# Kernel tuning notes

Hardware: AMD Instinct MI355X
Metric: run time of the kernel (lower is better)

Reference implementation:

```python
import jax, jax.numpy as jnp
import numpy as np

EPS = 1e-12

def setup_inputs() -> dict:
    key = jax.random.key(0)
    k1, k2, k3, k4, k5 = jax.random.split(key, 5)
    n, C, B = 8, 1024, 2048
    X = jax.random.normal(k1, (n, C, B), dtype=jnp.float32)
    # xavier_uniform bound for square [C, C] weight
    bound = float(np.sqrt(6.0 / (C + C)))
    Wk_w = jax.random.uniform(k2, (C, C), dtype=jnp.float32, minval=-bound, maxval=bound)
    Wq_w = jax.random.uniform(k3, (C, C), dtype=jnp.float32, minval=-bound, maxval=bound)
    # nn.Linear default bias init: U(-1/sqrt(C), 1/sqrt(C))
    bb = 1.0 / float(np.sqrt(C))
    Wk_b = jax.random.uniform(k4, (C,), dtype=jnp.float32, minval=-bb, maxval=bb)
    Wq_b = jax.random.uniform(k5, (C,), dtype=jnp.float32, minval=-bb, maxval=bb)
    return {"X": X, "Wk_w": Wk_w, "Wk_b": Wk_b, "Wq_w": Wq_w, "Wq_b": Wq_b}

def reference(X, Wk_w, Wk_b, Wq_w, Wq_b):
    # X: [n, C, B]; weights: [C, C]; biases: [C]
    K = jnp.einsum('oc,ncb->nob', Wk_w, X) + Wk_b[:, None]   # [n, C, B]
    Q = jnp.einsum('oc,ncb->nob', Wq_w, X) + Wq_b[:, None]   # [n, C, B]
    DK2 = jnp.sum(K * K, axis=1)                              # [n, B]
    DQ2 = jnp.sum(Q * Q, axis=1)                              # [n, B]
    DQK = jnp.sqrt(jnp.maximum(DQ2[:, :, None] * DK2[:, None, :], EPS))  # [n, B, B]
    Y = jnp.einsum('ncb,nck->nbk', Q, K) / DQK                # [n, B, B] cosine-like scores
    SM = jax.nn.softmax(Y, axis=1)                            # softmax over query axis (dim=1)
    Z = jnp.einsum('ncb,nbk->nck', X, SM)                     # [n, C, B]
    return Z
```

## Files before the change

kernel.cpp:

```cpp
#include <hip/hip_runtime.h>
#include <hip/hip_bf16.h>

typedef __bf16 v8bf __attribute__((ext_vector_type(8)));
typedef __bf16 v4bf __attribute__((ext_vector_type(4)));
typedef float  v4f  __attribute__((ext_vector_type(4)));

#define AS1 __attribute__((address_space(1)))
#define AS3 __attribute__((address_space(3)))

static __device__ __forceinline__ void gload_lds16(const void* g, void* l) {
  __builtin_amdgcn_global_load_lds((const AS1 void*)g, (AS3 void*)l, 16, 0, 0);
}

__global__ __launch_bounds__(256)
void cvt_bf16(const float* __restrict__ in, __bf16* __restrict__ out, long n) {
  const long i = ((long)blockIdx.x * 256 + threadIdx.x) * 4;
  if (i >= n) return;
  v4f v = *(const v4f*)&in[i];
  v4bf o;
#pragma unroll
  for (int u = 0; u < 4; ++u) o[u] = (__bf16)v[u];
  *(v4bf*)&out[i] = o;
}

__global__ __launch_bounds__(256)
void cvt_transpose(const float* __restrict__ X, __bf16* __restrict__ XT) {
  __shared__ float t[64][65];
  const int b0 = blockIdx.x * 64, c0 = blockIdx.y * 64;
  const long n = blockIdx.z;
  const float* Xp = X + n * (1024L * 2048);
  __bf16* Tp = XT + n * (2048L * 1024);
  const int tid = threadIdx.x;
  const int r16 = tid >> 4, c4 = (tid & 15) * 4;
#pragma unroll
  for (int it = 0; it < 4; ++it) {
    const int r = r16 + it * 16;
    *(v4f*)&t[r][c4] = *(const v4f*)&Xp[(long)(c0 + r) * 2048 + b0 + c4];
  }
  __syncthreads();
  const int rb8 = tid >> 3, c8 = (tid & 7) * 8;
#pragma unroll
  for (int it = 0; it < 2; ++it) {
    const int rb = rb8 + it * 32;
    v8bf o;
#pragma unroll
    for (int u = 0; u < 8; ++u) o[u] = (__bf16)t[c8 + u][rb];
    *(v8bf*)&Tp[(long)(b0 + rb) * 1024 + c0 + c8] = o;
  }
}

#define BAR __builtin_amdgcn_s_barrier()
#define LGKM0 do { asm volatile("s_waitcnt lgkmcnt(0)" ::: "memory"); \
                   __builtin_amdgcn_sched_barrier(0); } while (0)
#define VMW6 do { asm volatile("s_waitcnt vmcnt(6)" ::: "memory"); \
                  __builtin_amdgcn_sched_barrier(0); } while (0)
#define VMW0 do { asm volatile("s_waitcnt vmcnt(0)" ::: "memory"); \
                  __builtin_amdgcn_sched_barrier(0); } while (0)
#define MM(HM, HN) do { \
  __builtin_amdgcn_s_setprio(1); \
  _Pragma("unroll") for (int ks = 0; ks < 2; ++ks) \
  _Pragma("unroll") for (int u = 0; u < 2; ++u) \
  _Pragma("unroll") for (int j = 0; j < 4; ++j) \
    acc[2 * (HM) + u][4 * (HN) + j] = __builtin_amdgcn_mfma_f32_16x16x32_bf16( \
        af[u][ks], bfr[j][ks], acc[2 * (HM) + u][4 * (HN) + j], 0, 0, 0); \
  __builtin_amdgcn_s_setprio(0); } while (0)

template<int KD, int EPI, typename OT>
__global__ __launch_bounds__(512, 2)
void gemm256(const __bf16* __restrict__ Abase, const __bf16* __restrict__ Bbase,
             OT* __restrict__ Obase, const __bf16* __restrict__ bias,
             const float* __restrict__ dk2, const float* __restrict__ dq2,
             long sA, long sB, long sO) {
  __shared__ __align__(128) __bf16 lds[65536];

  const int tid = threadIdx.x;
  const int wave = tid >> 6, lane = tid & 63;
  const int qr = wave >> 1, qc = wave & 1;
  const int fr = lane & 15, q = lane >> 4;
  const int f7 = fr & 7;

  const int n0 = blockIdx.x * 256, m0 = blockIdx.y * 256;
  const long z = blockIdx.z;

  const __bf16* A = Abase + z * sA + (long)m0 * KD;
  const __bf16* B = Bbase + z * sB + (long)n0 * KD;

  const int lrow = wave * 16 + (lane >> 3);
  const int lchunk = ((lane & 7) ^ (lane >> 3)) << 3;
  const __bf16* Alane = A + (long)lrow * KD + lchunk;
  const __bf16* Blane = B + (long)lrow * KD + lchunk;
  const int dbase = wave * 1024;

  auto stage = [&](int kt, int isB, int half) {
    const __bf16* gp = (isB ? Blane : Alane) + (long)(half * 128) * KD + kt * 64;
    __bf16* dp = lds + (kt & 1) * 32768 + isB * 16384 + half * 8192 + dbase;
    gload_lds16(gp, dp);
    gload_lds16(gp + (long)8 * KD, dp + 512);
  };

  v4f acc[4][8];
#pragma unroll
  for (int i = 0; i < 4; ++i)
#pragma unroll
    for (int j = 0; j < 8; ++j) acc[i][j] = {0.f, 0.f, 0.f, 0.f};

  v8bf af[2][2], bfr[4][2];
  auto readA = [&](const __bf16* sa, int hm) {
#pragma unroll
    for (int u = 0; u < 2; ++u) {
      const int rb = (hm * 128 + qr * 32 + u * 16 + fr) * 64;
      af[u][0] = *(const v8bf*)&sa[rb + ((q ^ f7) << 3)];
      af[u][1] = *(const v8bf*)&sa[rb + (((q | 4) ^ f7) << 3)];
    }
  };
  auto readB = [&](const __bf16* sb, int hn) {
#pragma unroll
    for (int j = 0; j < 4; ++j) {
      const int rb = (hn * 128 + qc * 64 + j * 16 + fr) * 64;
      bfr[j][0] = *(const v8bf*)&sb[rb + ((q ^ f7) << 3)];
      bfr[j][1] = *(const v8bf*)&sb[rb + (((q | 4) ^ f7) << 3)];
    }
  };

  constexpr int NT = KD / 64;
  constexpr int NI = NT / 2;
  __bf16* s0 = lds;
  __bf16* s1 = lds + 32768;

  stage(0, 0, 0); stage(0, 1, 0); stage(0, 1, 1); stage(0, 0, 1);
  stage(1, 0, 0); stage(1, 1, 1); stage(1, 0, 1);
  VMW6; BAR;

#pragma unroll 1
  for (int m = 0; m < NI; ++m) {
    const int T1 = 2 * m + 1, T2 = 2 * m + 2, T3 = 2 * m + 3;
    const bool nl = (m != NI - 1);
    readA(s0, 0); readB(s0 + 16384, 0);
    stage(T1, 1, 0);
    BAR; LGKM0; MM(0, 0); BAR;
    readB(s0 + 16384, 1);
    if (nl) stage(T2, 0, 0);
    BAR; LGKM0; MM(0, 1); BAR;
    readA(s0, 1);
    if (nl) stage(T2, 1, 1);
    BAR; LGKM0; MM(1, 1); BAR;
    readB(s0 + 16384, 0);
    if (nl) stage(T2, 0, 1);
    BAR; LGKM0; MM(1, 0);
    if (nl) { VMW6; } else { VMW0; }
    BAR;
    readA(s1, 0); readB(s1 + 16384, 0);
    if (nl) stage(T2, 1, 0);
    BAR; LGKM0; MM(0, 0); BAR;
    readB(s1 + 16384, 1);
    if (nl) stage(T3, 0, 0);
    BAR; LGKM0; MM(0, 1); BAR;
    readA(s1, 1);
    if (nl) stage(T3, 1, 1);
    BAR; LGKM0; MM(1, 1); BAR;
    readB(s1 + 16384, 0);
    if (nl) stage(T3, 0, 1);
    BAR; LGKM0; MM(1, 0);
    if (nl) { VMW6; } else { VMW0; }
    BAR;
  }

  OT* O = Obase + z * sO;
  const int ldo = gridDim.x * 256;
#pragma unroll
  for (int bj = 0; bj < 8; ++bj) {
    const int col = n0 + (bj >> 2) * 128 + qc * 64 + (bj & 3) * 16 + fr;
    float cv = 0.f;
    if (EPI == 0) cv = (float)bias[col];
    if (EPI == 1) cv = dq2[z * 2048 + col];
#pragma unroll
    for (int ai = 0; ai < 4; ++ai) {
      const int row0 = m0 + (ai >> 1) * 128 + qr * 32 + (ai & 1) * 16 + q * 4;
#pragma unroll
      for (int r = 0; r < 4; ++r) {
        float v = acc[ai][bj][r];
        const int row = row0 + r;
        if (EPI == 0) v = fminf(fmaxf(v + cv, -32.f), 32.f);
        if (EPI == 1) {
          v *= rsqrtf(fmaxf(dk2[z * 2048 + row] * cv, 1e-12f));
          v = fminf(fmaxf(v, -4.f), 4.f);
        }
        if (EPI == 2) v = fminf(fmaxf(v, -1.f), 1.f);
        O[(long)row * ldo + col] = (OT)v;
      }
    }
  }
}

__global__ __launch_bounds__(256)
void rownorm2(const __bf16* __restrict__ T, float* __restrict__ out) {
  const int tid = threadIdx.x;
  const long row = (long)blockIdx.y * gridDim.x + blockIdx.x;
  const __bf16* p = T + row * 1024;
  v4bf v = *(const v4bf*)&p[tid * 4];
  float s = 0.f;
#pragma unroll
  for (int u = 0; u < 4; ++u) { float f = (float)v[u]; s += f * f; }
#pragma unroll
  for (int off = 32; off > 0; off >>= 1) s += __shfl_down(s, off);
  __shared__ float red[4];
  if ((tid & 63) == 0) red[tid >> 6] = s;
  __syncthreads();
  if (tid == 0) out[row] = red[0] + red[1] + red[2] + red[3];
}

__global__ __launch_bounds__(256)
void softmax_rows(__bf16* __restrict__ Y) {
  const int tid = threadIdx.x;
  const long row = (long)blockIdx.y * gridDim.x + blockIdx.x;
  __bf16* p = Y + row * 2048;
  v8bf v = *(const v8bf*)&p[tid * 8];
  float f[8];
  float s = 0.f;
#pragma unroll
  for (int u = 0; u < 8; ++u) { f[u] = __expf((float)v[u]); s += f[u]; }
#pragma unroll
  for (int off = 32; off > 0; off >>= 1) s += __shfl_down(s, off);
  __shared__ float red[4];
  __shared__ float stot;
  if ((tid & 63) == 0) red[tid >> 6] = s;
  __syncthreads();
  if (tid == 0) stot = 1.f / (red[0] + red[1] + red[2] + red[3]);
  __syncthreads();
  const float inv = stot;
  v8bf o;
#pragma unroll
  for (int u = 0; u < 8; ++u) o[u] = (__bf16)(f[u] * inv);
  *(v8bf*)&p[tid * 8] = o;
}

extern "C" void kernel_launch(void* const* d_in, const int* in_sizes, int n_in,
                              void* d_out, int out_size, void* d_ws, size_t ws_size,
                              hipStream_t stream) {
  const float* X    = (const float*)d_in[0];
  const float* Wk_w = (const float*)d_in[1];
  const float* Wk_b = (const float*)d_in[2];
  const float* Wq_w = (const float*)d_in[3];
  const float* Wq_b = (const float*)d_in[4];
  float* out = (float*)d_out;

  char* ws = (char*)d_ws;
  __bf16* XT  = (__bf16*)(ws);
  __bf16* Xbf = (__bf16*)(ws);
  __bf16* YT  = (__bf16*)(ws + 33554432L);
  char* aux   = ws + 100663296L;
  float*  DK2   = (float*)(aux);
  float*  DQ2   = (float*)(aux + 65536L);
  __bf16* Wk_bf = (__bf16*)(aux + 131072L);
  __bf16* Wq_bf = (__bf16*)(aux + 131072L + 2097152L);
  __bf16* bk_bf = (__bf16*)(aux + 131072L + 4194304L);
  __bf16* bq_bf = (__bf16*)(aux + 131072L + 4196352L);
  __bf16* KT = (__bf16*)d_out;
  __bf16* QT = (__bf16*)((char*)d_out + 33554432L);

  cvt_bf16<<<1024, 256, 0, stream>>>(Wk_w, Wk_bf, 1048576L);
  cvt_bf16<<<1024, 256, 0, stream>>>(Wq_w, Wq_bf, 1048576L);
  cvt_bf16<<<1, 256, 0, stream>>>(Wk_b, bk_bf, 1024L);
  cvt_bf16<<<1, 256, 0, stream>>>(Wq_b, bq_bf, 1024L);
  cvt_transpose<<<dim3(32, 16, 8), 256, 0, stream>>>(X, XT);
  gemm256<1024, 0, __bf16><<<dim3(4, 8, 8), 512, 0, stream>>>(
      XT, Wk_bf, KT, bk_bf, nullptr, nullptr, 2048L * 1024, 0L, 2048L * 1024);
  gemm256<1024, 0, __bf16><<<dim3(4, 8, 8), 512, 0, stream>>>(
      XT, Wq_bf, QT, bq_bf, nullptr, nullptr, 2048L * 1024, 0L, 2048L * 1024);
  cvt_bf16<<<16384, 256, 0, stream>>>(X, Xbf, 16777216L);
  rownorm2<<<dim3(2048, 8), 256, 0, stream>>>(KT, DK2);
  rownorm2<<<dim3(2048, 8), 256, 0, stream>>>(QT, DQ2);
  gemm256<1024, 1, __bf16><<<dim3(8, 8, 8), 512, 0, stream>>>(
      KT, QT, YT, nullptr, DK2, DQ2, 2048L * 1024, 2048L * 1024, 2048L * 2048);
  softmax_rows<<<dim3(2048, 8), 256, 0, stream>>>(YT);
  gemm256<2048, 2, float><<<dim3(8, 4, 8), 512, 0, stream>>>(
      Xbf, YT, out, nullptr, nullptr, nullptr, 1024L * 2048, 2048L * 2048, 1024L * 2048);
}
```

Measured before the change: 404.7 us.

## Fuse row norms into projection GEMM epilogue with vectorized stores and XCD block remap

Deletes the two rownorm2 kernels. The K and Q projection GEMM epilogues now compute per-row sums of squares and add them into zeroed DK2/DQ2 buffers with shuffle reductions and atomicAdd. MFMA operands are swapped so each lane holds four consecutive columns, which allows 4-wide vector stores and vector loads of bias and dq2. Blocks are also remapped in an XCD-aware interleaved order, and the LDS pipeline is reordered to put the wait ahead of each barrier and drop the trailing barriers. The intent is to remove two full passes over K and Q plus scattered scalar stores, at the cost of atomic contention, norms taken from fp32 values rather than bf16-rounded ones, and a riskier barrier schedule.

```diff
diff --git a/kernel.cpp b/kernel.cpp
--- a/kernel.cpp
+++ b/kernel.cpp
@@ -21,6 +21,13 @@
 #pragma unroll
   for (int u = 0; u < 4; ++u) o[u] = (__bf16)v[u];
   *(v4bf*)&out[i] = o;
+}
+
+__global__ __launch_bounds__(256)
+void zero_f32(float* __restrict__ p, long n) {
+  const long i = ((long)blockIdx.x * 256 + threadIdx.x) * 4;
+  if (i >= n) return;
+  *(v4f*)&p[i] = v4f{0.f, 0.f, 0.f, 0.f};
 }
 
 __global__ __launch_bounds__(256)
@@ -52,24 +59,22 @@
 #define BAR __builtin_amdgcn_s_barrier()
 #define LGKM0 do { asm volatile("s_waitcnt lgkmcnt(0)" ::: "memory"); \
                    __builtin_amdgcn_sched_barrier(0); } while (0)
-#define VMW6 do { asm volatile("s_waitcnt vmcnt(6)" ::: "memory"); \
-                  __builtin_amdgcn_sched_barrier(0); } while (0)
-#define VMW0 do { asm volatile("s_waitcnt vmcnt(0)" ::: "memory"); \
-                  __builtin_amdgcn_sched_barrier(0); } while (0)
+#define VMW(N) do { asm volatile("s_waitcnt vmcnt(" #N ")" ::: "memory"); \
+                    __builtin_amdgcn_sched_barrier(0); } while (0)
 #define MM(HM, HN) do { \
   __builtin_amdgcn_s_setprio(1); \
   _Pragma("unroll") for (int ks = 0; ks < 2; ++ks) \
   _Pragma("unroll") for (int u = 0; u < 2; ++u) \
   _Pragma("unroll") for (int j = 0; j < 4; ++j) \
     acc[2 * (HM) + u][4 * (HN) + j] = __builtin_amdgcn_mfma_f32_16x16x32_bf16( \
-        af[u][ks], bfr[j][ks], acc[2 * (HM) + u][4 * (HN) + j], 0, 0, 0); \
+        bfr[j][ks], af[u][ks], acc[2 * (HM) + u][4 * (HN) + j], 0, 0, 0); \
   __builtin_amdgcn_s_setprio(0); } while (0)
 
 template<int KD, int EPI, typename OT>
 __global__ __launch_bounds__(512, 2)
 void gemm256(const __bf16* __restrict__ Abase, const __bf16* __restrict__ Bbase,
              OT* __restrict__ Obase, const __bf16* __restrict__ bias,
-             const float* __restrict__ dk2, const float* __restrict__ dq2,
+             float* __restrict__ dk2, const float* __restrict__ dq2,
              long sA, long sB, long sO) {
   __shared__ __align__(128) __bf16 lds[65536];
 
@@ -79,9 +84,16 @@
   const int fr = lane & 15, q = lane >> 4;
   const int f7 = fr & 7;
 
-  const int n0 = blockIdx.x * 256, m0 = blockIdx.y * 256;
-  const long z = blockIdx.z;
-
+  const int gx = gridDim.x, gy = gridDim.y;
+  int id = blockIdx.x + gx * (blockIdx.y + gy * blockIdx.z);
+  const int chunk = (gx * gy * gridDim.z) >> 3;
+  id = (id & 7) * chunk + (id >> 3);
+  const int bx = id % gx;
+  const int rem = id / gx;
+  const int by = rem % gy;
+  const long z = rem / gy;
+
+  const int n0 = bx * 256, m0 = by * 256;
   const __bf16* A = Abase + z * sA + (long)m0 * KD;
   const __bf16* B = Bbase + z * sB + (long)n0 * KD;
 
@@ -127,86 +139,99 @@
   __bf16* s0 = lds;
   __bf16* s1 = lds + 32768;
 
-  stage(0, 0, 0); stage(0, 1, 0); stage(0, 1, 1); stage(0, 0, 1);
-  stage(1, 0, 0); stage(1, 1, 1); stage(1, 0, 1);
-  VMW6; BAR;
+  stage(0, 0, 0); stage(0, 1, 0); stage(0, 0, 1); stage(0, 1, 1);
+  stage(1, 1, 0); stage(1, 0, 1); stage(1, 1, 1);
+  VMW(6); BAR;
 
 #pragma unroll 1
   for (int m = 0; m < NI; ++m) {
-    const int T1 = 2 * m + 1, T2 = 2 * m + 2, T3 = 2 * m + 3;
     const bool nl = (m != NI - 1);
+    const int t1 = 2 * m + 1, t2 = 2 * m + 2, t3 = 2 * m + 3;
     readA(s0, 0); readB(s0 + 16384, 0);
-    stage(T1, 1, 0);
-    BAR; LGKM0; MM(0, 0); BAR;
+    stage(t1, 0, 0);
+    LGKM0; BAR; MM(0, 0);
+    readA(s0, 1);
+    if (nl) stage(t2, 1, 0);
+    LGKM0; BAR; MM(1, 0);
     readB(s0 + 16384, 1);
-    if (nl) stage(T2, 0, 0);
-    BAR; LGKM0; MM(0, 1); BAR;
-    readA(s0, 1);
-    if (nl) stage(T2, 1, 1);
-    BAR; LGKM0; MM(1, 1); BAR;
-    readB(s0 + 16384, 0);
-    if (nl) stage(T2, 0, 1);
-    BAR; LGKM0; MM(1, 0);
-    if (nl) { VMW6; } else { VMW0; }
-    BAR;
+    if (nl) stage(t2, 0, 1);
+    LGKM0; BAR; MM(1, 1);
+    readA(s0, 0);
+    if (nl) stage(t2, 1, 1);
+    LGKM0;
+    if (nl) { VMW(6); } else { VMW(0); }
+    BAR; MM(0, 1);
     readA(s1, 0); readB(s1 + 16384, 0);
-    if (nl) stage(T2, 1, 0);
-    BAR; LGKM0; MM(0, 0); BAR;
+    if (nl) stage(t2, 0, 0);
+    LGKM0; BAR; MM(0, 0);
+    readA(s1, 1);
+    if (nl) stage(t3, 1, 0);
+    LGKM0; BAR; MM(1, 0);
     readB(s1 + 16384, 1);
-    if (nl) stage(T3, 0, 0);
-    BAR; LGKM0; MM(0, 1); BAR;
-    readA(s1, 1);
-    if (nl) stage(T3, 1, 1);
-    BAR; LGKM0; MM(1, 1); BAR;
-    readB(s1 + 16384, 0);
-    if (nl) stage(T3, 0, 1);
-    BAR; LGKM0; MM(1, 0);
-    if (nl) { VMW6; } else { VMW0; }
-    BAR;
+    if (nl) stage(t3, 0, 1);
+    LGKM0; BAR; MM(1, 1);
+    readA(s1, 0);
+    if (nl) stage(t3, 1, 1);
+    LGKM0;
+    if (nl) { VMW(6); } else { VMW(0); }
+    BAR; MM(0, 1);
   }
 
   OT* O = Obase + z * sO;
-  const int ldo = gridDim.x * 256;
-#pragma unroll
-  for (int bj = 0; bj < 8; ++bj) {
-    const int col = n0 + (bj >> 2) * 128 + qc * 64 + (bj & 3) * 16 + fr;
-    float cv = 0.f;
-    if (EPI == 0) cv = (float)bias[col];
-    if (EPI == 1) cv = dq2[z * 2048 + col];
-#pragma unroll
-    for (int ai = 0; ai < 4; ++ai) {
-      const int row0 = m0 + (ai >> 1) * 128 + qr * 32 + (ai & 1) * 16 + q * 4;
+  const int ldo = gx * 256;
+#pragma unroll
+  for (int ai = 0; ai < 4; ++ai) {
+    const int row = m0 + (ai >> 1) * 128 + qr * 32 + (ai & 1) * 16 + fr;
+    float rk = 0.f;
+    if (EPI == 1) rk = dk2[z * 2048 + row];
+    float rs = 0.f;
+#pragma unroll
+    for (int bj = 0; bj < 8; ++bj) {
+      const int colb = n0 + (bj >> 2) * 128 + qc * 64 + (bj & 3) * 16 + q * 4;
+      float cv[4];
+      if (EPI == 0) {
+        v4bf bb = *(const v4bf*)&bias[colb];
+#pragma unroll
+        for (int r = 0; r < 4; ++r) cv[r] = (float)bb[r];
+      }
+      if (EPI == 1) {
+        v4f dd = *(const v4f*)&dq2[z * 2048 + colb];
+#pragma unroll
+        for (int r = 0; r < 4; ++r) cv[r] = dd[r];
+      }
+      float vv[4];
 #pragma unroll
       for (int r = 0; r < 4; ++r) {
         float v = acc[ai][bj][r];
-        const int row = row0 + r;
-        if (EPI == 0) v = fminf(fmaxf(v + cv, -32.f), 32.f);
+        if (EPI == 0) {
+          v = fminf(fmaxf(v + cv[r], -32.f), 32.f);
+          rs += v * v;
+        }
         if (EPI == 1) {
-          v *= rsqrtf(fmaxf(dk2[z * 2048 + row] * cv, 1e-12f));
+          v *= rsqrtf(fmaxf(rk * cv[r], 1e-12f));
           v = fminf(fmaxf(v, -4.f), 4.f);
         }
         if (EPI == 2) v = fminf(fmaxf(v, -1.f), 1.f);
-        O[(long)row * ldo + col] = (OT)v;
+        vv[r] = v;
+      }
+      if (sizeof(OT) == 2) {
+        v4bf o;
+#pragma unroll
+        for (int r = 0; r < 4; ++r) o[r] = (__bf16)vv[r];
+        *(v4bf*)&O[(long)row * ldo + colb] = o;
+      } else {
+        v4f o;
+#pragma unroll
+        for (int r = 0; r < 4; ++r) o[r] = vv[r];
+        *(v4f*)&O[(long)row * ldo + colb] = o;
       }
     }
+    if (EPI == 0) {
+      rs += __shfl_xor(rs, 16);
+      rs += __shfl_xor(rs, 32);
+      if (q == 0) atomicAdd(&dk2[z * 2048 + row], rs);
+    }
   }
-}
-
-__global__ __launch_bounds__(256)
-void rownorm2(const __bf16* __restrict__ T, float* __restrict__ out) {
-  const int tid = threadIdx.x;
-  const long row = (long)blockIdx.y * gridDim.x + blockIdx.x;
-  const __bf16* p = T + row * 1024;
-  v4bf v = *(const v4bf*)&p[tid * 4];
-  float s = 0.f;
-#pragma unroll
-  for (int u = 0; u < 4; ++u) { float f = (float)v[u]; s += f * f; }
-#pragma unroll
-  for (int off = 32; off > 0; off >>= 1) s += __shfl_down(s, off);
-  __shared__ float red[4];
-  if ((tid & 63) == 0) red[tid >> 6] = s;
-  __syncthreads();
-  if (tid == 0) out[row] = red[0] + red[1] + red[2] + red[3];
 }
 
 __global__ __launch_bounds__(256)
@@ -262,14 +287,13 @@
   cvt_bf16<<<1024, 256, 0, stream>>>(Wq_w, Wq_bf, 1048576L);
   cvt_bf16<<<1, 256, 0, stream>>>(Wk_b, bk_bf, 1024L);
   cvt_bf16<<<1, 256, 0, stream>>>(Wq_b, bq_bf, 1024L);
+  zero_f32<<<32, 256, 0, stream>>>(DK2, 32768L);
   cvt_transpose<<<dim3(32, 16, 8), 256, 0, stream>>>(X, XT);
   gemm256<1024, 0, __bf16><<<dim3(4, 8, 8), 512, 0, stream>>>(
-      XT, Wk_bf, KT, bk_bf, nullptr, nullptr, 2048L * 1024, 0L, 2048L * 1024);
+      XT, Wk_bf, KT, bk_bf, DK2, nullptr, 2048L * 1024, 0L, 2048L * 1024);
   gemm256<1024, 0, __bf16><<<dim3(4, 8, 8), 512, 0, stream>>>(
-      XT, Wq_bf, QT, bq_bf, nullptr, nullptr, 2048L * 1024, 0L, 2048L * 1024);
+      XT, Wq_bf, QT, bq_bf, DQ2, nullptr, 2048L * 1024, 0L, 2048L * 1024);
   cvt_bf16<<<16384, 256, 0, stream>>>(X, Xbf, 16777216L);
-  rownorm2<<<dim3(2048, 8), 256, 0, stream>>>(KT, DK2);
-  rownorm2<<<dim3(2048, 8), 256, 0, stream>>>(QT, DQ2);
   gemm256<1024, 1, __bf16><<<dim3(8, 8, 8), 512, 0, stream>>>(
       KT, QT, YT, nullptr, DK2, DQ2, 2048L * 1024, 2048L * 1024, 2048L * 2048);
   softmax_rows<<<dim3(2048, 8), 256, 0, stream>>>(YT);
```

After: 366.7 us. 9.4% less time.
